# Optimization experiments

Measured on AMD Instinct MI355X. Metric: run time of the kernel, lower is better.

The kernel has to match this reference:

```python
import jax, jax.numpy as jnp
import numpy as np

EPS = 1e-5

def layernorm(x, gamma, beta):
    # torch.var default is unbiased (ddof=1) - faithful to source
    m = jnp.mean(x, axis=-1, keepdims=True)
    d = x.shape[-1]
    var = jnp.sum((x - m) ** 2, axis=-1, keepdims=True) / (d - 1)
    return gamma * (x - m) / jnp.sqrt(var + EPS) + beta

def setup_inputs() -> dict:
    key = jax.random.key(0)
    B, S, D, H = 8, 1024, 768, 12
    hd = D // H
    ks = jax.random.split(key, 20)
    s_in = 1.0 / np.sqrt(D)
    s_ff = 1.0 / np.sqrt(4 * D)
    return {
        "x":  jax.random.normal(ks[0], (B, S, D), jnp.float32),
        "Wq": jax.random.uniform(ks[1], (H, D, hd), jnp.float32, -s_in, s_in),
        "bq": jax.random.uniform(ks[2], (H, hd), jnp.float32, -s_in, s_in),
        "Wk": jax.random.uniform(ks[3], (H, D, hd), jnp.float32, -s_in, s_in),
        "bk": jax.random.uniform(ks[4], (H, hd), jnp.float32, -s_in, s_in),
        "Wv": jax.random.uniform(ks[5], (H, D, hd), jnp.float32, -s_in, s_in),
        "bv": jax.random.uniform(ks[6], (H, hd), jnp.float32, -s_in, s_in),
        "Wo": jax.random.uniform(ks[7], (D, D), jnp.float32, -s_in, s_in),
        "bo": jax.random.uniform(ks[8], (D,), jnp.float32, -s_in, s_in),
        "W1": jax.random.uniform(ks[9], (D, 4 * D), jnp.float32, -s_in, s_in),
        "b1": jax.random.uniform(ks[10], (4 * D,), jnp.float32, -s_in, s_in),
        "W2": jax.random.uniform(ks[11], (4 * D, D), jnp.float32, -s_ff, s_ff),
        "b2": jax.random.uniform(ks[12], (D,), jnp.float32, -s_ff, s_ff),
        "g1": jnp.ones((D,), jnp.float32),
        "be1": jnp.zeros((D,), jnp.float32),
        "g2": jnp.ones((D,), jnp.float32),
        "be2": jnp.zeros((D,), jnp.float32),
    }

def reference(x, Wq, bq, Wk, bk, Wv, bv, Wo, bo, W1, b1, W2, b2, g1, be1, g2, be2):
    # x = ln1(x); x = x + mha(x); x = ln2(x); out = x + ffwd(x)
    x = layernorm(x, g1, be1)
    hd = Wq.shape[-1]
    q = jnp.einsum('bsd,hdk->bhsk', x, Wq) + bq[None, :, None, :]
    k = jnp.einsum('bsd,hdk->bhsk', x, Wk) + bk[None, :, None, :]
    v = jnp.einsum('bsd,hdk->bhsk', x, Wv) + bv[None, :, None, :]
    att = jnp.einsum('bhqk,bhsk->bhqs', q, k) * (hd ** -0.5)
    att = jax.nn.softmax(att, axis=-1)
    o = jnp.einsum('bhqs,bhsk->bhqk', att, v)  # [B,H,S,hd]
    B, H, S, _ = o.shape
    o = jnp.transpose(o, (0, 2, 1, 3)).reshape(B, S, H * hd)  # concat heads
    x = x + o @ Wo + bo
    x = layernorm(x, g2, be2)
    h = jax.nn.gelu(x @ W1 + b1, approximate=False)
    out = x + h @ W2 + b2
    return out
```

## Files before the change

kernel.cpp:

```cpp
#include <hip/hip_runtime.h>
#include <stdint.h>

typedef __attribute__((ext_vector_type(8))) short bf16x8;
typedef __attribute__((ext_vector_type(4))) float f32x4;

#define GPTR(p) ((const __attribute__((address_space(1))) void*)(p))
#define LPTR(p) ((__attribute__((address_space(3))) void*)(p))

__device__ __forceinline__ float b2f(unsigned short u) {
  union { unsigned int i; float f; } v; v.i = ((unsigned int)u) << 16; return v.f;
}
__device__ __forceinline__ unsigned short f2b(float f) {
  union { float f; unsigned int i; } v; v.f = f;
  unsigned int i = v.i;
  return (unsigned short)((i + 0x7FFFu + ((i >> 16) & 1u)) >> 16);
}

__global__ __launch_bounds__(256) void ln_kernel(const unsigned short* __restrict__ xin,
                                                 const float* __restrict__ g,
                                                 const float* __restrict__ be,
                                                 unsigned short* __restrict__ y) {
  const int D = 768;
  int row = blockIdx.x;
  int t = threadIdx.x;
  float v[3];
  float s = 0.f, s2 = 0.f;
#pragma unroll
  for (int i = 0; i < 3; ++i) {
    int c = t + i * 256;
    float f = b2f(xin[(size_t)row * D + c]);
    v[i] = f; s += f; s2 += f * f;
  }
#pragma unroll
  for (int d = 32; d > 0; d >>= 1) { s += __shfl_down(s, d); s2 += __shfl_down(s2, d); }
  __shared__ float red[8];
  int w = t >> 6;
  if ((t & 63) == 0) { red[w] = s; red[4 + w] = s2; }
  __syncthreads();
  s = red[0] + red[1] + red[2] + red[3];
  s2 = red[4] + red[5] + red[6] + red[7];
  float mean = s * (1.0f / 768.0f);
  float var = (s2 - 768.0f * mean * mean) * (1.0f / 767.0f);
  float rstd = rsqrtf(var + 1e-5f);
  unsigned short* yr = y + (size_t)row * D;
#pragma unroll
  for (int i = 0; i < 3; ++i) {
    int c = t + i * 256;
    yr[c] = f2b((v[i] - mean) * rstd * g[c] + be[c]);
  }
}

__global__ __launch_bounds__(256) void prep_kernel(const float* __restrict__ Wq,
                                                   const float* __restrict__ Wk,
                                                   const float* __restrict__ Wv,
                                                   const float* __restrict__ Wo,
                                                   const float* __restrict__ W1,
                                                   const float* __restrict__ W2,
                                                   const float* __restrict__ x,
                                                   const float* __restrict__ g1,
                                                   const float* __restrict__ be1,
                                                   unsigned short* __restrict__ Wqkvt,
                                                   unsigned short* __restrict__ Wot,
                                                   unsigned short* __restrict__ W1t,
                                                   unsigned short* __restrict__ W2t,
                                                   unsigned short* __restrict__ y) {
  int bid = blockIdx.x;
  int t = threadIdx.x;
  if (bid < 6912) {
    __shared__ float tile[32][33];
    const float* in; unsigned short* out; int R, C, c0, r0;
    if (bid < 1728) {
      int seg = bid / 576, r = bid % 576;
      int z = r / 48, t2 = r % 48, bx = t2 & 1, by = t2 >> 1;
      in = (seg == 0 ? Wq : seg == 1 ? Wk : Wv) + (size_t)z * 768 * 64;
      out = Wqkvt + (size_t)seg * 768 * 768 + (size_t)z * 64 * 768;
      R = 768; C = 64; c0 = bx * 32; r0 = by * 32;
    } else if (bid < 2304) {
      int r = bid - 1728, bx = r % 24, by = r / 24;
      in = Wo; out = Wot; R = 768; C = 768; c0 = bx * 32; r0 = by * 32;
    } else if (bid < 4608) {
      int r = bid - 2304, bx = r % 96, by = r / 96;
      in = W1; out = W1t; R = 768; C = 3072; c0 = bx * 32; r0 = by * 32;
    } else {
      int r = bid - 4608, bx = r % 24, by = r / 24;
      in = W2; out = W2t; R = 3072; C = 768; c0 = bx * 32; r0 = by * 32;
    }
    int tc = t & 31, tr = t >> 5;
#pragma unroll
    for (int i = 0; i < 4; ++i) {
      int r = tr + i * 8;
      tile[r][tc] = in[(size_t)(r0 + r) * C + c0 + tc];
    }
    __syncthreads();
#pragma unroll
    for (int i = 0; i < 4; ++i) {
      int r = tr + i * 8;
      out[(size_t)(c0 + r) * R + r0 + tc] = f2b(tile[tc][r]);
    }
  } else {
    const int D = 768;
    int row = bid - 6912;
    float v[3];
    float s = 0.f, s2 = 0.f;
#pragma unroll
    for (int i = 0; i < 3; ++i) {
      int c = t + i * 256;
      float f = x[(size_t)row * D + c];
      v[i] = f; s += f; s2 += f * f;
    }
#pragma unroll
    for (int d = 32; d > 0; d >>= 1) { s += __shfl_down(s, d); s2 += __shfl_down(s2, d); }
    __shared__ float red[8];
    int w = t >> 6;
    if ((t & 63) == 0) { red[w] = s; red[4 + w] = s2; }
    __syncthreads();
    s = red[0] + red[1] + red[2] + red[3];
    s2 = red[4] + red[5] + red[6] + red[7];
    float mean = s * (1.0f / 768.0f);
    float var = (s2 - 768.0f * mean * mean) * (1.0f / 767.0f);
    float rstd = rsqrtf(var + 1e-5f);
    unsigned short* yr = y + (size_t)row * D;
#pragma unroll
    for (int i = 0; i < 3; ++i) {
      int c = t + i * 256;
      yr[c] = f2b((v[i] - mean) * rstd * g1[c] + be1[c]);
    }
  }
}

template <int EPI, int TM, int TN>
__global__ __launch_bounds__(256) void gemm_bt(const unsigned short* __restrict__ A,
                                               const unsigned short* __restrict__ Bt,
                                               int M, int N, int K,
                                               const float* __restrict__ bias0,
                                               const float* __restrict__ bias1,
                                               const float* __restrict__ bias2,
                                               const unsigned short* __restrict__ res,
                                               unsigned short* __restrict__ out0,
                                               unsigned short* __restrict__ out1,
                                               unsigned short* __restrict__ out2,
                                               float* __restrict__ outf) {
  const int II = TM / 32, JJ = TN / 32;
  __shared__ unsigned short As[2][TM * 32];
  __shared__ unsigned short Bs[2][TN * 32];
  int t = threadIdx.x;
  int n0 = blockIdx.x * TN, m0 = blockIdx.y * TM;
  int lane = t & 63, w = t >> 6;
  int lr = lane & 15, quad = lane >> 4;
  int wm = (w >> 1) * (TM / 2), wn = (w & 1) * (TN / 2);
  int rowInWave = lane >> 2;
  int colq = (lane & 3) * 8;
  f32x4 zero4 = {0.f, 0.f, 0.f, 0.f};
  f32x4 acc[II][JJ];
#pragma unroll
  for (int i = 0; i < II; ++i)
#pragma unroll
    for (int j = 0; j < JJ; ++j) acc[i][j] = zero4;
  for (int k0 = 0; k0 < K; k0 += 64) {
    __syncthreads();
#pragma unroll
    for (int s = 0; s < 2; ++s) {
#pragma unroll
      for (int rnd = 0; rnd < TM / 64; ++rnd) {
        int rbase = rnd * 64 + w * 16;
        int row = rbase + rowInWave;
        __builtin_amdgcn_global_load_lds(GPTR(A + (size_t)(m0 + row) * K + k0 + s * 32 + colq),
                                         LPTR(&As[s][rbase * 32]), 16, 0, 0);
      }
#pragma unroll
      for (int rnd = 0; rnd < TN / 64; ++rnd) {
        int rbase = rnd * 64 + w * 16;
        int row = rbase + rowInWave;
        __builtin_amdgcn_global_load_lds(GPTR(Bt + (size_t)(n0 + row) * K + k0 + s * 32 + colq),
                                         LPTR(&Bs[s][rbase * 32]), 16, 0, 0);
      }
    }
    __syncthreads();
#pragma unroll
    for (int s = 0; s < 2; ++s) {
      bf16x8 af[II];
#pragma unroll
      for (int i = 0; i < II; ++i)
        af[i] = *(const bf16x8*)(&As[s][(wm + i * 16 + lr) * 32 + quad * 8]);
#pragma unroll
      for (int j = 0; j < JJ; ++j) {
        bf16x8 bfr = *(const bf16x8*)(&Bs[s][(wn + j * 16 + lr) * 32 + quad * 8]);
#pragma unroll
        for (int i = 0; i < II; ++i)
          acc[i][j] = __builtin_amdgcn_mfma_f32_16x16x32_bf16(af[i], bfr, acc[i][j], 0, 0, 0);
      }
    }
  }
#pragma unroll
  for (int i = 0; i < II; ++i) {
#pragma unroll
    for (int j = 0; j < JJ; ++j) {
#pragma unroll
      for (int r = 0; r < 4; ++r) {
        int rg = m0 + wm + i * 16 + quad * 4 + r;
        int cg = n0 + wn + j * 16 + lr;
        float val = acc[i][j][r];
        if (EPI == 1) {
          int b = rg >> 10, sx = rg & 1023;
          if (cg < 768) {
            int h = cg >> 6, kk = cg & 63;
            out0[(((size_t)(b * 12 + h) << 10) + sx) * 64 + kk] = f2b(val + bias0[cg]);
          } else if (cg < 1536) {
            int cc = cg - 768, h = cc >> 6, kk = cc & 63;
            out1[(((size_t)(b * 12 + h) << 10) + sx) * 64 + kk] = f2b(val + bias1[cc]);
          } else {
            int cc = cg - 1536, h = cc >> 6, kk = cc & 63;
            out2[((size_t)(b * 12 + h) << 16) + ((size_t)kk << 10) + sx] = f2b(val + bias2[cc]);
          }
        } else if (EPI == 2) {
          val += bias0[cg] + b2f(res[(size_t)rg * N + cg]);
          out0[(size_t)rg * N + cg] = f2b(val);
        } else if (EPI == 3) {
          float xg = val + bias0[cg];
          val = 0.5f * xg * (1.0f + erff(xg * 0.70710678118654752f));
          out0[(size_t)rg * N + cg] = f2b(val);
        } else if (EPI == 4) {
          outf[(size_t)rg * N + cg] = val + bias0[cg] + b2f(res[(size_t)rg * N + cg]);
        }
      }
    }
  }
}

__global__ __launch_bounds__(256) void attn_kernel(const unsigned short* __restrict__ q,
                                                   const unsigned short* __restrict__ k,
                                                   const unsigned short* __restrict__ vt,
                                                   unsigned short* __restrict__ out) {
  __shared__ unsigned short Ks[64 * 72];
  __shared__ unsigned short Vs[64 * 72];
  __shared__ unsigned short Ps[4][32 * 72];
  int bh = blockIdx.y;
  int q0 = blockIdx.x * 128;
  int t = threadIdx.x, lane = t & 63, w = t >> 6;
  int lr = lane & 15, quad = lane >> 4;
  const unsigned short* qb = q + (size_t)bh * 1024 * 64;
  const unsigned short* kb = k + (size_t)bh * 1024 * 64;
  const unsigned short* vb = vt + (size_t)bh * 64 * 1024;
  bf16x8 aq[2][2];
#pragma unroll
  for (int i = 0; i < 2; ++i)
#pragma unroll
    for (int ks = 0; ks < 2; ++ks)
      aq[i][ks] = *(const bf16x8*)(qb + (size_t)(q0 + w * 32 + i * 16 + lr) * 64 + ks * 32 + quad * 8);
  f32x4 zero4 = {0.f, 0.f, 0.f, 0.f};
  f32x4 oacc[2][4];
  float l_part[2][4];
#pragma unroll
  for (int i = 0; i < 2; ++i)
#pragma unroll
    for (int j = 0; j < 4; ++j) oacc[i][j] = zero4;
#pragma unroll
  for (int i = 0; i < 2; ++i)
#pragma unroll
    for (int r = 0; r < 4; ++r) l_part[i][r] = 0.f;
  int srow = t >> 3, spart = t & 7;
  unsigned short* ps = &Ps[w][0];
  for (int st = 0; st < 16; ++st) {
    int s0 = st * 64;
    __syncthreads();
#pragma unroll
    for (int rnd = 0; rnd < 2; ++rnd) {
      int rr = rnd * 32 + srow;
      *(uint4*)(&Ks[rr * 72 + spart * 8]) = *(const uint4*)(kb + (size_t)(s0 + rr) * 64 + spart * 8);
      *(uint4*)(&Vs[rr * 72 + spart * 8]) = *(const uint4*)(vb + (size_t)rr * 1024 + s0 + spart * 8);
    }
    __syncthreads();
#pragma unroll
    for (int i = 0; i < 2; ++i) {
#pragma unroll
      for (int j = 0; j < 4; ++j) {
        bf16x8 bk0 = *(const bf16x8*)(&Ks[(j * 16 + lr) * 72 + quad * 8]);
        bf16x8 bk1 = *(const bf16x8*)(&Ks[(j * 16 + lr) * 72 + 32 + quad * 8]);
        f32x4 z = zero4;
        z = __builtin_amdgcn_mfma_f32_16x16x32_bf16(aq[i][0], bk0, z, 0, 0, 0);
        z = __builtin_amdgcn_mfma_f32_16x16x32_bf16(aq[i][1], bk1, z, 0, 0, 0);
#pragma unroll
        for (int r = 0; r < 4; ++r) {
          float p = __expf(z[r] * 0.125f);
          l_part[i][r] += p;
          ps[(i * 16 + quad * 4 + r) * 72 + j * 16 + lr] = f2b(p);
        }
      }
    }
    __syncthreads();
#pragma unroll
    for (int i = 0; i < 2; ++i) {
#pragma unroll
      for (int ks = 0; ks < 2; ++ks) {
        bf16x8 ap = *(const bf16x8*)(&ps[(i * 16 + lr) * 72 + ks * 32 + quad * 8]);
#pragma unroll
        for (int j = 0; j < 4; ++j) {
          bf16x8 bv = *(const bf16x8*)(&Vs[(j * 16 + lr) * 72 + ks * 32 + quad * 8]);
          oacc[i][j] = __builtin_amdgcn_mfma_f32_16x16x32_bf16(ap, bv, oacc[i][j], 0, 0, 0);
        }
      }
    }
  }
  int b = bh / 12, h = bh % 12;
#pragma unroll
  for (int i = 0; i < 2; ++i) {
#pragma unroll
    for (int r = 0; r < 4; ++r) {
      float l = l_part[i][r];
#pragma unroll
      for (int d = 1; d < 16; d <<= 1) l += __shfl_xor(l, d);
      float inv = 1.0f / l;
      int sx = q0 + w * 32 + i * 16 + quad * 4 + r;
      size_t base = ((size_t)(b * 1024 + sx)) * 768 + h * 64;
#pragma unroll
      for (int j = 0; j < 4; ++j)
        out[base + j * 16 + lr] = f2b(oacc[i][j][r] * inv);
    }
  }
}

extern "C" void kernel_launch(void* const* d_in, const int* in_sizes, int n_in,
                              void* d_out, int out_size, void* d_ws, size_t ws_size,
                              hipStream_t stream) {
  const float* x  = (const float*)d_in[0];
  const float* Wq = (const float*)d_in[1];
  const float* bq = (const float*)d_in[2];
  const float* Wk = (const float*)d_in[3];
  const float* bk = (const float*)d_in[4];
  const float* Wv = (const float*)d_in[5];
  const float* bv = (const float*)d_in[6];
  const float* Wo = (const float*)d_in[7];
  const float* bo = (const float*)d_in[8];
  const float* W1 = (const float*)d_in[9];
  const float* b1 = (const float*)d_in[10];
  const float* W2 = (const float*)d_in[11];
  const float* b2 = (const float*)d_in[12];
  const float* g1 = (const float*)d_in[13];
  const float* be1= (const float*)d_in[14];
  const float* g2 = (const float*)d_in[15];
  const float* be2= (const float*)d_in[16];
  float* outf = (float*)d_out;

  const size_t SLOT = (size_t)8192 * 768;
  unsigned short* ws = (unsigned short*)d_ws;
  unsigned short* Wqkvt = ws;
  unsigned short* Wot   = Wqkvt + (size_t)2304 * 768;
  unsigned short* W1t   = Wot   + (size_t)768 * 768;
  unsigned short* W2t   = W1t   + (size_t)3072 * 768;
  unsigned short* s0    = W2t   + (size_t)768 * 3072;
  unsigned short* s1    = s0 + SLOT;
  unsigned short* s2    = s1 + SLOT;
  unsigned short* s3    = s2 + SLOT;
  unsigned short* s4    = s3 + SLOT;

  unsigned short* qbuf = s0;
  unsigned short* kbuf = s1;
  unsigned short* y    = s2;
  unsigned short* x2   = s3;
  unsigned short* ao   = s4;
  unsigned short* y2   = s4;
  unsigned short* hb   = s0;
  unsigned short* vtb  = (unsigned short*)d_out;

  prep_kernel<<<6912 + 8192, 256, 0, stream>>>(Wq, Wk, Wv, Wo, W1, W2, x, g1, be1,
                                               Wqkvt, Wot, W1t, W2t, y);

  gemm_bt<1, 128, 128><<<dim3(18, 64), 256, 0, stream>>>(y, Wqkvt, 8192, 2304, 768,
                                               bq, bk, bv, nullptr, qbuf, kbuf, vtb, nullptr);
  attn_kernel<<<dim3(8, 96), 256, 0, stream>>>(qbuf, kbuf, vtb, ao);
  gemm_bt<2, 64, 64><<<dim3(12, 128), 256, 0, stream>>>(ao, Wot, 8192, 768, 768,
                                              bo, nullptr, nullptr, y, x2, nullptr, nullptr, nullptr);
  ln_kernel<<<8192, 256, 0, stream>>>(x2, g2, be2, y2);
  gemm_bt<3, 128, 128><<<dim3(24, 64), 256, 0, stream>>>(y2, W1t, 8192, 3072, 768,
                                               b1, nullptr, nullptr, nullptr, hb, nullptr, nullptr, nullptr);
  gemm_bt<4, 64, 64><<<dim3(12, 128), 256, 0, stream>>>(hb, W2t, 8192, 768, 3072,
                                              b2, nullptr, nullptr, y2, nullptr, nullptr, nullptr, outf);
}
```

Before: 453.7 us.

## Double-buffer GEMM LDS tiles with prefetch and enlarge output-projection/FFN2 tiles

Restructures the bf16 GEMM main loop so the global-to-LDS load of the next 32-wide K slice is issued into the alternate buffer before computing on the current one. This uses one barrier per iteration instead of two, and aims to overlap memory latency with MFMA work. Separately, the Wo and W2 GEMMs switch from 64x64 to 128x128 tiles to increase data reuse per block. The larger tiles cut those grids to 384 blocks, which may underfill the GPU. The loop also issues one redundant load on the final iteration.

```diff
diff --git a/kernel.cpp b/kernel.cpp
--- a/kernel.cpp
+++ b/kernel.cpp
@@ -156,39 +156,48 @@
   for (int i = 0; i < II; ++i)
 #pragma unroll
     for (int j = 0; j < JJ; ++j) acc[i][j] = zero4;
-  for (int k0 = 0; k0 < K; k0 += 64) {
-    __syncthreads();
-#pragma unroll
-    for (int s = 0; s < 2; ++s) {
-#pragma unroll
-      for (int rnd = 0; rnd < TM / 64; ++rnd) {
-        int rbase = rnd * 64 + w * 16;
-        int row = rbase + rowInWave;
-        __builtin_amdgcn_global_load_lds(GPTR(A + (size_t)(m0 + row) * K + k0 + s * 32 + colq),
-                                         LPTR(&As[s][rbase * 32]), 16, 0, 0);
-      }
-#pragma unroll
-      for (int rnd = 0; rnd < TN / 64; ++rnd) {
-        int rbase = rnd * 64 + w * 16;
-        int row = rbase + rowInWave;
-        __builtin_amdgcn_global_load_lds(GPTR(Bt + (size_t)(n0 + row) * K + k0 + s * 32 + colq),
-                                         LPTR(&Bs[s][rbase * 32]), 16, 0, 0);
-      }
-    }
-    __syncthreads();
-#pragma unroll
-    for (int s = 0; s < 2; ++s) {
-      bf16x8 af[II];
+
+  const int niter = K >> 5;
+#pragma unroll
+  for (int rnd = 0; rnd < TM / 64; ++rnd) {
+    int rbase = rnd * 64 + w * 16;
+    __builtin_amdgcn_global_load_lds(GPTR(A + (size_t)(m0 + rbase + rowInWave) * K + colq),
+                                     LPTR(&As[0][rbase * 32]), 16, 0, 0);
+  }
+#pragma unroll
+  for (int rnd = 0; rnd < TN / 64; ++rnd) {
+    int rbase = rnd * 64 + w * 16;
+    __builtin_amdgcn_global_load_lds(GPTR(Bt + (size_t)(n0 + rbase + rowInWave) * K + colq),
+                                     LPTR(&Bs[0][rbase * 32]), 16, 0, 0);
+  }
+  for (int it = 0; it < niter; ++it) {
+    __syncthreads();
+    int cur = it & 1, nxt = cur ^ 1;
+    int kn = (it + 1 < niter ? it + 1 : it) << 5;
+#pragma unroll
+    for (int rnd = 0; rnd < TM / 64; ++rnd) {
+      int rbase = rnd * 64 + w * 16;
+      __builtin_amdgcn_global_load_lds(GPTR(A + (size_t)(m0 + rbase + rowInWave) * K + kn + colq),
+                                       LPTR(&As[nxt][rbase * 32]), 16, 0, 0);
+    }
+#pragma unroll
+    for (int rnd = 0; rnd < TN / 64; ++rnd) {
+      int rbase = rnd * 64 + w * 16;
+      __builtin_amdgcn_global_load_lds(GPTR(Bt + (size_t)(n0 + rbase + rowInWave) * K + kn + colq),
+                                       LPTR(&Bs[nxt][rbase * 32]), 16, 0, 0);
+    }
+    const unsigned short* as_ = &As[cur][0];
+    const unsigned short* bs_ = &Bs[cur][0];
+    bf16x8 af[II];
+#pragma unroll
+    for (int i = 0; i < II; ++i)
+      af[i] = *(const bf16x8*)(&as_[(wm + i * 16 + lr) * 32 + quad * 8]);
+#pragma unroll
+    for (int j = 0; j < JJ; ++j) {
+      bf16x8 bfr = *(const bf16x8*)(&bs_[(wn + j * 16 + lr) * 32 + quad * 8]);
 #pragma unroll
       for (int i = 0; i < II; ++i)
-        af[i] = *(const bf16x8*)(&As[s][(wm + i * 16 + lr) * 32 + quad * 8]);
-#pragma unroll
-      for (int j = 0; j < JJ; ++j) {
-        bf16x8 bfr = *(const bf16x8*)(&Bs[s][(wn + j * 16 + lr) * 32 + quad * 8]);
-#pragma unroll
-        for (int i = 0; i < II; ++i)
-          acc[i][j] = __builtin_amdgcn_mfma_f32_16x16x32_bf16(af[i], bfr, acc[i][j], 0, 0, 0);
-      }
+        acc[i][j] = __builtin_amdgcn_mfma_f32_16x16x32_bf16(af[i], bfr, acc[i][j], 0, 0, 0);
     }
   }
 #pragma unroll
@@ -368,11 +377,11 @@
   gemm_bt<1, 128, 128><<<dim3(18, 64), 256, 0, stream>>>(y, Wqkvt, 8192, 2304, 768,
                                                bq, bk, bv, nullptr, qbuf, kbuf, vtb, nullptr);
   attn_kernel<<<dim3(8, 96), 256, 0, stream>>>(qbuf, kbuf, vtb, ao);
-  gemm_bt<2, 64, 64><<<dim3(12, 128), 256, 0, stream>>>(ao, Wot, 8192, 768, 768,
+  gemm_bt<2, 128, 128><<<dim3(6, 64), 256, 0, stream>>>(ao, Wot, 8192, 768, 768,
                                               bo, nullptr, nullptr, y, x2, nullptr, nullptr, nullptr);
   ln_kernel<<<8192, 256, 0, stream>>>(x2, g2, be2, y2);
   gemm_bt<3, 128, 128><<<dim3(24, 64), 256, 0, stream>>>(y2, W1t, 8192, 3072, 768,
                                                b1, nullptr, nullptr, nullptr, hb, nullptr, nullptr, nullptr);
-  gemm_bt<4, 64, 64><<<dim3(12, 128), 256, 0, stream>>>(hb, W2t, 8192, 768, 3072,
+  gemm_bt<4, 128, 128><<<dim3(6, 64), 256, 0, stream>>>(hb, W2t, 8192, 768, 3072,
                                               b2, nullptr, nullptr, y2, nullptr, nullptr, nullptr, outf);
 }
```

Result: faster. 439.1 us (-3.2%).
